# Optimization experiments

Hardware: AMD Instinct MI355X
Metric: run time of the kernel (lower is better)

The kernel has to match this reference:

```python
import jax, jax.numpy as jnp
import numpy as np

TEMP = 0.7
TOPK_RATIO = 0.75
BN_EPS = 1e-5  # eval-mode BN with running_mean=0, running_var=1


def conv3x3(x, w):
    # x: [N,C,H,W], w: [O,I,3,3], stride 1, pad 1
    return jax.lax.conv_general_dilated(x, w, (1, 1), 'SAME',
                                        dimension_numbers=('NCHW', 'OIHW', 'NCHW'))


def bn(x, g, b):
    scale = g / jnp.sqrt(1.0 + BN_EPS)
    return x * scale[:, None, None] + b[:, None, None]


def glu(x):
    c = x.shape[1] // 2
    return x[:, :c] * jax.nn.sigmoid(x[:, c:])


def resblock(x, w1, g1, b1, w2, g2, b2):
    out = glu(bn(conv3x3(x, w1), g1, b1))
    out = bn(conv3x3(out, w2), g2, b2)
    return out + x


def refined_attention(h_code, word_embs, w_ctx, mask):
    B, C, H, W = h_code.shape
    Q = H * W
    S = word_embs.shape[2]
    # conv_context is a 1x1 conv (no bias): pure channel projection
    sourceT = jnp.einsum('oc,bcs->bos', w_ctx, word_embs)   # [B, idf, S]
    target = h_code.reshape(B, C, Q)                        # [B, idf, Q]
    attn = jnp.einsum('bcq,bcs->bqs', target, sourceT)      # [B, Q, S]
    attn = attn.reshape(B * Q, S) / TEMP
    # faithful to torch: mask.repeat(queryL, 1) tiles mask over rows
    mask_exp = jnp.tile(mask, (Q, 1))                       # [B*Q, S]
    attn = jnp.where(mask_exp, -jnp.inf, attn)
    if TOPK_RATIO < 1.0 and S > 1:
        k = max(1, int(S * TOPK_RATIO))
        topk_vals, _ = jax.lax.top_k(attn, k)               # sorted desc
        threshold = topk_vals[:, -1:]                       # min of top-k
        attn = jnp.where(attn < threshold, -jnp.inf, attn)
    p = jax.nn.softmax(attn, axis=1)
    nan_rows = jnp.any(jnp.isnan(p), axis=1, keepdims=True)
    p = jnp.where(nan_rows, 1.0 / S, p)                     # uniform fallback
    p = p.reshape(B, Q, S)
    attn_t = jnp.swapaxes(p, 1, 2)                          # [B, S, Q]
    wctx = jnp.einsum('bos,bsq->boq', sourceT, attn_t).reshape(B, C, H, W)
    att_map = attn_t.reshape(B, S, H, W)
    return wctx, att_map


def upsample2x(x):
    return jnp.repeat(jnp.repeat(x, 2, axis=2), 2, axis=3)


def reference(h_code, c_code, word_embs, w_ctx,
              r0_w1, r0_g1, r0_b1, r0_w2, r0_g2, r0_b2,
              r1_w1, r1_g1, r1_b1, r1_w2, r1_g2, r1_b2,
              up_w, up_g, up_b, mask):
    # c_code is in the signature of NEXT_STAGE_G.forward but unused (as in AttnGAN)
    c_code_att, att = refined_attention(h_code, word_embs, w_ctx, mask)
    h_c = jnp.concatenate([h_code, c_code_att], axis=1)     # [B, 2*ngf, H, W]
    out = resblock(h_c, r0_w1, r0_g1, r0_b1, r0_w2, r0_g2, r0_b2)
    out = resblock(out, r1_w1, r1_g1, r1_b1, r1_w2, r1_g2, r1_b2)
    # upBlock: nearest upsample x2 -> conv3x3(2ngf, 2ngf) -> BN -> GLU -> ngf
    out = glu(bn(conv3x3(upsample2x(out), up_w), up_g, up_b))
    return out, att


def setup_inputs() -> dict:
    key = jax.random.key(0)
    ks = jax.random.split(key, 24)
    B, ngf, H, W = 8, 64, 128, 128
    nef, ncf, S = 256, 100, 32
    C2 = 2 * ngf  # 128
    std = 0.02
    inp = {
        'h_code': jax.random.normal(ks[0], (B, ngf, H, W), jnp.float32),
        'c_code': jax.random.normal(ks[1], (B, ncf), jnp.float32),
        'word_embs': jax.random.normal(ks[2], (B, nef, S), jnp.float32),
        'mask': jax.random.randint(ks[3], (B, S), 0, 2).astype(bool),
        'w_ctx': jax.random.normal(ks[4], (ngf, nef), jnp.float32) * std,
    }
    for i, base in enumerate([5, 11]):
        inp[f'r{i}_w1'] = jax.random.normal(ks[base + 0], (2 * C2, C2, 3, 3), jnp.float32) * std
        inp[f'r{i}_g1'] = jnp.ones((2 * C2,), jnp.float32)
        inp[f'r{i}_b1'] = jnp.zeros((2 * C2,), jnp.float32)
        inp[f'r{i}_w2'] = jax.random.normal(ks[base + 3], (C2, C2, 3, 3), jnp.float32) * std
        inp[f'r{i}_g2'] = jnp.ones((C2,), jnp.float32)
        inp[f'r{i}_b2'] = jnp.zeros((C2,), jnp.float32)
    inp['up_w'] = jax.random.normal(ks[17], (2 * ngf, C2, 3, 3), jnp.float32) * std
    inp['up_g'] = jnp.ones((2 * ngf,), jnp.float32)
    inp['up_b'] = jnp.zeros((2 * ngf,), jnp.float32)
    return inp
```

## Files before the change

kernel.cpp:

```cpp
#include <hip/hip_runtime.h>
#include <math.h>


#define B_N 8
#define NGF 64
#define HC 128
#define WC 128
#define QN (HC*WC)
#define NEF 256
#define SN 32
#define TEMP_INV (1.0f/0.7f)
#define BN_SC 0.99999500003749969f
#define TOPK 24

typedef _Float16 f16;
typedef __attribute__((ext_vector_type(8))) _Float16 f16x8;
typedef __attribute__((ext_vector_type(4))) _Float16 f16x4;
typedef __attribute__((ext_vector_type(4))) float f32x4;

__device__ __forceinline__ void gload16(const void* g, void* l) {
    __builtin_amdgcn_global_load_lds(
        (const __attribute__((address_space(1))) void*)g,
        (__attribute__((address_space(3))) void*)l,
        16, 0, 0);
}

__global__ void prep_mask_k(const void* __restrict__ mraw,
                            unsigned* __restrict__ mbits,
                            unsigned* __restrict__ zp) {
    __shared__ int mode;
    if (threadIdx.x == 0) {
        const unsigned* u = (const unsigned*)mraw;
        bool i32 = true, f32m = true;
        for (int i = 0; i < 64; ++i) {
            unsigned v = u[i];
            if (v > 1u) i32 = false;
            if (v != 0u && v != 0x3F800000u) f32m = false;
        }
        mode = i32 ? 0 : (f32m ? 1 : 2);
    }
    __syncthreads();
    int t = threadIdx.x;
    if (t < 64) zp[t] = 0u;
    if (t < B_N) {
        unsigned bits = 0;
        for (int s = 0; s < SN; ++s) {
            int idx = t * SN + s;
            bool on;
            if (mode == 0)      on = ((const int*)mraw)[idx] != 0;
            else if (mode == 1) on = ((const float*)mraw)[idx] != 0.0f;
            else                on = ((const unsigned char*)mraw)[idx] != 0;
            if (on) bits |= (1u << s);
        }
        mbits[t] = bits;
    }
}

__global__ __launch_bounds__(256) void source_t_k(
        const float* __restrict__ w_ctx, const float* __restrict__ word_embs,
        float* __restrict__ sT) {
    int b = blockIdx.x >> 3;
    int o = ((blockIdx.x & 7) << 3) + (threadIdx.x >> 5);
    int s = threadIdx.x & 31;
    const float* wrow = w_ctx + (size_t)o * NEF;
    const float* wb = word_embs + (size_t)b * NEF * SN + s;
    float acc = 0.0f;
    #pragma unroll 8
    for (int c = 0; c < NEF; ++c) acc += wrow[c] * wb[(size_t)c * SN];
    sT[((size_t)b * NGF + o) * SN + s] = acc;
}

__global__ __launch_bounds__(256) void attention_k(
        const float* __restrict__ h_code, const float* __restrict__ sT,
        const unsigned* __restrict__ mbits,
        float* __restrict__ att_out,
        f16* __restrict__ hc) {
    int r0 = blockIdx.x * 256;
    int b = r0 >> 14;
    __shared__ float st[NGF * SN];
    const float* stg = sT + (size_t)b * NGF * SN;
    for (int i = threadIdx.x; i < NGF * SN; i += 256) st[i] = stg[i];
    __syncthreads();
    int q = (r0 & (QN - 1)) + threadIdx.x;

    const float* hb = h_code + (size_t)b * NGF * QN + q;
    f16* hcb = hc + ((size_t)b * QN + q) * 128;

    float a[SN];
    #pragma unroll
    for (int s = 0; s < SN; ++s) a[s] = 0.0f;
    for (int c0 = 0; c0 < NGF; c0 += 4) {
        float v[4];
        f16x4 t;
        #pragma unroll
        for (int r = 0; r < 4; ++r) {
            v[r] = hb[(size_t)(c0 + r) * QN];
            t[r] = (f16)v[r];
            #pragma unroll
            for (int s = 0; s < SN; ++s) a[s] += v[r] * st[(c0 + r) * SN + s];
        }
        *(f16x4*)(hcb + c0) = t;
    }
    unsigned mb = mbits[q & 7];
    #pragma unroll
    for (int s = 0; s < SN; ++s)
        a[s] = ((mb >> s) & 1u) ? -INFINITY : a[s] * TEMP_INV;

    float thr = -INFINITY;
    #pragma unroll
    for (int s = 0; s < SN; ++s) {
        int rank = 0;
        #pragma unroll
        for (int j = 0; j < SN; ++j)
            rank += (a[j] > a[s]) || (a[j] == a[s] && j < s);
        if (rank == TOPK - 1) thr = a[s];
    }
    float m = -INFINITY;
    #pragma unroll
    for (int s = 0; s < SN; ++s) {
        if (a[s] < thr) a[s] = -INFINITY;
        m = fmaxf(m, a[s]);
    }
    float p[SN];
    if (m == -INFINITY) {
        #pragma unroll
        for (int s = 0; s < SN; ++s) p[s] = 1.0f / SN;
    } else {
        float sum = 0.0f;
        #pragma unroll
        for (int s = 0; s < SN; ++s) { p[s] = __expf(a[s] - m); sum += p[s]; }
        float inv = 1.0f / sum;
        #pragma unroll
        for (int s = 0; s < SN; ++s) p[s] *= inv;
    }
    float* ao = att_out + (size_t)b * SN * QN + q;
    #pragma unroll
    for (int s = 0; s < SN; ++s) ao[(size_t)s * QN] = p[s];
    for (int c0 = 0; c0 < NGF; c0 += 4) {
        f16x4 t;
        #pragma unroll
        for (int r = 0; r < 4; ++r) {
            float acc = 0.0f;
            #pragma unroll
            for (int s = 0; s < SN; ++s) acc += st[(c0 + r) * SN + s] * p[s];
            t[r] = (f16)acc;
        }
        *(f16x4*)(hcb + 64 + c0) = t;
    }
}

__global__ __launch_bounds__(256) void wt_transform_k(
        const float* __restrict__ w, f16* __restrict__ wt,
        int total, int HALF ) {
    int idx = blockIdx.x * 256 + threadIdx.x;
    if (idx >= total) return;
    int e   = idx & 7;
    int gp  = (idx >> 3) & 3;
    int cop = (idx >> 5) & 63;
    int u   = idx >> 11;
    int t   = u % 9;
    int v   = u / 9;
    int cc  = v & 3;
    int cb  = v >> 2;
    int g   = gp ^ ((cop >> 1) & 3);
    int ci  = cc * 32 + g * 8 + e;
    int co  = HALF ? (cop < 32 ? cb * 32 + cop : HALF + cb * 32 + (cop - 32))
                   : cb * 64 + cop;
    wt[idx] = (f16)w[((size_t)co * 128 + ci) * 9 + t];
}

__global__ __launch_bounds__(256) void wt_up_transform_k(
        const float* __restrict__ w, f16* __restrict__ wt) {
    int idx = blockIdx.x * 256 + threadIdx.x;
    int e   = idx & 7;
    int gp  = (idx >> 3) & 3;
    int cop = (idx >> 5) & 63;
    int tap = (idx >> 11) & 3;
    int pw  = (idx >> 13) & 1;
    int cc  = (idx >> 14) & 3;
    int ph  = (idx >> 16) & 1;
    int cb  = (idx >> 17) & 1;
    int g   = gp ^ ((cop >> 1) & 3);
    int ci  = cc * 32 + g * 8 + e;
    int co  = cop < 32 ? cb * 32 + cop : 64 + cb * 32 + (cop - 32);
    int ra = tap >> 1, bb = tap & 1;
    const float* wp = w + ((size_t)co * 128 + ci) * 9;
    float acc = 0.0f;
    #pragma unroll
    for (int kh = 0; kh < 3; ++kh) {
        int rma = (ph == 0) ? (kh == 0 ? 0 : 1) : (kh == 2 ? 1 : 0);
        if (rma != ra) continue;
        #pragma unroll
        for (int kw = 0; kw < 3; ++kw) {
            int cma = (pw == 0) ? (kw == 0 ? 0 : 1) : (kw == 2 ? 1 : 0);
            if (cma == bb) acc += wp[kh * 3 + kw];
        }
    }
    wt[idx] = (f16)acc;
}

template<int COUT, bool GLU, bool RES, bool UP, int HOUT, int WOUT, bool FINAL>
__global__ __launch_bounds__(256) void conv_mfma_k(
        const f16* __restrict__ in, const f16* __restrict__ wt,
        const float* __restrict__ gamma, const float* __restrict__ beta,
        const f16* __restrict__ res, f16* __restrict__ outh,
        float* __restrict__ outf, const char* __restrict__ zeros) {
    constexpr int HALF = COUT / 2;
    constexpr int OCH  = GLU ? HALF : COUT;
    constexpr int HIN  = UP ? HOUT / 2 : HOUT;
    constexpr int WIN  = UP ? WOUT / 2 : WOUT;
    constexpr int RPT  = 256 / WOUT;
    constexpr int ROWS_IN = UP ? 2 : RPT + 2;
    constexpr int NIN_G   = ROWS_IN * 520;
    constexpr int NIN_IT  = (NIN_G + 255) / 256;
    constexpr int NIN_PAD = NIN_IT * 256;
    constexpr int NTAP    = UP ? 4 : 9;
    constexpr int WBYTES  = UP ? 32768 : 36864;
    constexpr int WIT     = WBYTES / 4096;

    __shared__ char smem[NIN_PAD * 16 + WBYTES];
    char* sW = smem + NIN_PAD * 16;

    const int tid = threadIdx.x, lane = tid & 63, wv = tid >> 6;
    const int l15 = lane & 15, kg = lane >> 4;
    const int b = blockIdx.z, cb = blockIdx.y, qt = blockIdx.x;
    const int q0 = qt * 256;
    const int h0 = q0 / WOUT;
    const int ph = UP ? (h0 & 1) : 0;
    const int p  = wv >> 1;
    const int jq = ((wv & 1) << 6) + l15;

    f32x4 acc[4][4];
    #pragma unroll
    for (int m = 0; m < 4; ++m)
        #pragma unroll
        for (int n = 0; n < 4; ++n) acc[m][n] = (f32x4){0.f, 0.f, 0.f, 0.f};

    const f16* inb = in + (size_t)b * HIN * WIN * 128;
    const char* wtb = UP
        ? (const char*)wt + (size_t)(cb * 2 + ph) * 131072
        : (const char*)wt + (size_t)cb * 147456;

    const char* srcK[NIN_IT];
    #pragma unroll
    for (int k = 0; k < NIN_IT; ++k) {
        int idx = (k << 8) + tid;
        int r = idx / 520;
        int rem = idx - r * 520;
        int wi = rem >> 2, gp = rem & 3;
        int g = gp ^ ((wi >> 1) & 3);
        const char* s = zeros;
        if (UP) {
            int sh = (h0 >> 1) + r - 1 + ph;
            int sw = wi - 1;
            if (r < 2 && (unsigned)sh < (unsigned)HIN && (unsigned)sw < (unsigned)WIN)
                s = (const char*)(inb + (((size_t)sh * WIN + sw) << 7) + g * 8);
        } else {
            int gh = h0 - 1 + r;
            int gw = wi - 1;
            if (r < ROWS_IN && (unsigned)gh < (unsigned)HOUT && (unsigned)gw < (unsigned)WOUT)
                s = (const char*)(inb + (((size_t)gh * WIN + gw) << 7) + g * 8);
        }
        srcK[k] = s;
    }
    const int dstB = (tid & 192) << 4;

    for (int cc = 0; cc < 4; ++cc) {
        #pragma unroll
        for (int k = 0; k < NIN_IT; ++k)
            gload16(srcK[k] + cc * 64, smem + (k << 12) + dstB);
        const char* wsrc = wtb + cc * WBYTES + (tid << 4);
        #pragma unroll
        for (int k = 0; k < WIT; ++k)
            gload16(wsrc + (k << 12), sW + (k << 12) + dstB);
        __syncthreads();

        #pragma unroll
        for (int t = 0; t < NTAP; ++t) {
            f16x8 af[4], bf[4];
            const int tapbase = UP ? ((p * 4 + t) << 12) : (t << 12);
            #pragma unroll
            for (int m = 0; m < 4; ++m) {
                int co = m * 16 + l15;
                af[m] = *(const f16x8*)(sW + tapbase + (co << 6)
                                        + ((kg ^ ((co >> 1) & 3)) << 4));
            }
            #pragma unroll
            for (int n = 0; n < 4; ++n) {
                int off;
                if (UP) {
                    int si = jq + (n << 4) + (t & 1) + p;
                    off = (t >> 1) * 8320 + si * 64 + ((kg ^ ((si >> 1) & 3)) << 4);
                } else {
                    const int kh = t / 3, kw = t % 3;
                    int row = (wv >> 1) + kh;
                    int wi = ((wv & 1) << 6) + (n << 4) + l15 + kw;
                    off = row * 8320 + wi * 64 + ((kg ^ ((wi >> 1) & 3)) << 4);
                }
                bf[n] = *(const f16x8*)(smem + off);
            }
            #pragma unroll
            for (int m = 0; m < 4; ++m)
                #pragma unroll
                for (int n = 0; n < 4; ++n)
                    acc[m][n] = __builtin_amdgcn_mfma_f32_16x16x32_f16(af[m], bf[n], acc[m][n], 0, 0, 0);
        }
        __syncthreads();
    }

    const int r4 = kg * 4;
    if (GLU) {
        #pragma unroll
        for (int mv = 0; mv < 2; ++mv) {
            const int v0 = cb * 32 + mv * 16 + r4;
            float s1[4], o1[4], s2[4], o2[4];
            #pragma unroll
            for (int r = 0; r < 4; ++r) {
                s1[r] = gamma[v0 + r] * BN_SC;        o1[r] = beta[v0 + r];
                s2[r] = gamma[v0 + r + HALF] * BN_SC; o2[r] = beta[v0 + r + HALF];
            }
            #pragma unroll
            for (int n = 0; n < 4; ++n) {
                float ov[4];
                #pragma unroll
                for (int r = 0; r < 4; ++r) {
                    float yv = acc[mv][n][r] * s1[r] + o1[r];
                    float zv = acc[mv + 2][n][r] * s2[r] + o2[r];
                    ov[r] = yv / (1.0f + __expf(-zv));
                }
                if (FINAL) {
                    const int w = UP ? 2 * (jq + (n << 4)) + p
                                     : ((wv << 6) + (n << 4) + l15) % WOUT;
                    const int h = UP ? h0 : h0 + ((wv << 6) + (n << 4) + l15) / WOUT;
                    #pragma unroll
                    for (int r = 0; r < 4; ++r)
                        outf[(((size_t)b * OCH + v0 + r) * HOUT + h) * WOUT + w] = ov[r];
                } else {
                    const int qc = (wv << 6) + (n << 4) + l15;
                    f16x4 tv;
                    #pragma unroll
                    for (int r = 0; r < 4; ++r) tv[r] = (f16)ov[r];
                    *(f16x4*)(outh + ((size_t)b * HOUT * WOUT + q0 + qc) * OCH + v0) = tv;
                }
            }
        }
    } else {
        #pragma unroll
        for (int m = 0; m < 4; ++m) {
            const int c0 = cb * 64 + m * 16 + r4;
            float s[4], o[4];
            #pragma unroll
            for (int r = 0; r < 4; ++r) {
                s[r] = gamma[c0 + r] * BN_SC; o[r] = beta[c0 + r];
            }
            #pragma unroll
            for (int n = 0; n < 4; ++n) {
                const int qc = (wv << 6) + (n << 4) + l15;
                const size_t pix = (size_t)b * HOUT * WOUT + q0 + qc;
                float ov[4];
                #pragma unroll
                for (int r = 0; r < 4; ++r) ov[r] = acc[m][n][r] * s[r] + o[r];
                if (RES) {
                    f16x4 rv = *(const f16x4*)(res + pix * 128 + c0);
                    #pragma unroll
                    for (int r = 0; r < 4; ++r) ov[r] += (float)rv[r];
                }
                f16x4 tv;
                #pragma unroll
                for (int r = 0; r < 4; ++r) tv[r] = (f16)ov[r];
                *(f16x4*)(outh + pix * OCH + c0) = tv;
            }
        }
    }
}

extern "C" void kernel_launch(void* const* d_in, const int* in_sizes, int n_in,
                              void* d_out, int out_size, void* d_ws, size_t ws_size,
                              hipStream_t stream) {
    (void)in_sizes; (void)n_in; (void)out_size; (void)ws_size;
    const float* h_code    = (const float*)d_in[0];
    const float* word_embs = (const float*)d_in[2];
    const void*  mask      = d_in[3];
    const float* w_ctx     = (const float*)d_in[4];
    const float* r0_w1 = (const float*)d_in[5];
    const float* r0_g1 = (const float*)d_in[6];
    const float* r0_b1 = (const float*)d_in[7];
    const float* r0_w2 = (const float*)d_in[8];
    const float* r0_g2 = (const float*)d_in[9];
    const float* r0_b2 = (const float*)d_in[10];
    const float* r1_w1 = (const float*)d_in[11];
    const float* r1_g1 = (const float*)d_in[12];
    const float* r1_b1 = (const float*)d_in[13];
    const float* r1_w2 = (const float*)d_in[14];
    const float* r1_g2 = (const float*)d_in[15];
    const float* r1_b2 = (const float*)d_in[16];
    const float* up_w  = (const float*)d_in[17];
    const float* up_g  = (const float*)d_in[18];
    const float* up_b  = (const float*)d_in[19];

    float* outp = (float*)d_out;
    float* attp = outp + (size_t)B_N * NGF * 4 * HC * WC;

    unsigned* mbits = (unsigned*)d_ws;
    char* zeros = (char*)d_ws + 256;
    float* sT  = (float*)((char*)d_ws + 1024);
    f16* hcA   = (f16*)((char*)d_ws + (size_t)(1 << 20));
    f16* wtbuf = (f16*)((char*)d_ws + (size_t)33 * (1 << 20));

    const int W1_TOT = 4 * 4 * 9 * 64 * 32;
    const int W2_TOT = 2 * 4 * 9 * 64 * 32;
    const int WUP_TOT = 2 * 2 * 4 * 2 * 4 * 64 * 32;
    f16* Wr0c1 = wtbuf;
    f16* Wr0c2 = Wr0c1 + W1_TOT;
    f16* Wr1c1 = Wr0c2 + W2_TOT;
    f16* Wr1c2 = Wr1c1 + W1_TOT;
    f16* Wup   = Wr1c2 + W2_TOT;

    f16* Bbuf = (f16*)d_out;
    f16* Cbuf = (f16*)((char*)d_out + ((size_t)32 << 20));

    prep_mask_k<<<1, 64, 0, stream>>>(mask, mbits, (unsigned*)zeros);
    source_t_k<<<64, 256, 0, stream>>>(w_ctx, word_embs, sT);

    wt_transform_k<<<(W1_TOT + 255) / 256, 256, 0, stream>>>(r0_w1, Wr0c1, W1_TOT, 128);
    wt_transform_k<<<(W2_TOT + 255) / 256, 256, 0, stream>>>(r0_w2, Wr0c2, W2_TOT, 0);
    wt_transform_k<<<(W1_TOT + 255) / 256, 256, 0, stream>>>(r1_w1, Wr1c1, W1_TOT, 128);
    wt_transform_k<<<(W2_TOT + 255) / 256, 256, 0, stream>>>(r1_w2, Wr1c2, W2_TOT, 0);
    wt_up_transform_k<<<WUP_TOT / 256, 256, 0, stream>>>(up_w, Wup);

    attention_k<<<(B_N * QN) / 256, 256, 0, stream>>>(h_code, sT, mbits, attp, hcA);

    conv_mfma_k<256, true,  false, false, 128, 128, false>
        <<<dim3(64, 4, B_N), 256, 0, stream>>>(hcA, Wr0c1, r0_g1, r0_b1, nullptr, Bbuf, nullptr, zeros);
    conv_mfma_k<128, false, true,  false, 128, 128, false>
        <<<dim3(64, 2, B_N), 256, 0, stream>>>(Bbuf, Wr0c2, r0_g2, r0_b2, hcA, Cbuf, nullptr, zeros);
    conv_mfma_k<256, true,  false, false, 128, 128, false>
        <<<dim3(64, 4, B_N), 256, 0, stream>>>(Cbuf, Wr1c1, r1_g1, r1_b1, nullptr, Bbuf, nullptr, zeros);
    conv_mfma_k<128, false, true,  false, 128, 128, false>
        <<<dim3(64, 2, B_N), 256, 0, stream>>>(Bbuf, Wr1c2, r1_g2, r1_b2, Cbuf, hcA, nullptr, zeros);
    conv_mfma_k<128, true,  false, true,  256, 256, true>
        <<<dim3(256, 2, B_N), 256, 0, stream>>>(hcA, Wup, up_g, up_b, nullptr, nullptr, outp, zeros);
}
```

Baseline: 455.2 us.

## Switch intermediate activations to channel-group-planar f16 layout

Activation buffers between the attention kernel and the convolution kernels move from pixel-major NHWC with 128 channels to a blocked layout: 16 planes of 8 channels, each plane pixel-contiguous. Conv input gathers now step between channel chunks by plane offsets instead of 64-byte offsets, and epilogue stores and residual reads use the new addressing. The zero-padding region is relocated and zeroed at strided offsets so it can serve the new cc stride. The goal is more contiguous, coalesced global accesses for the 16-byte LDS-direct loads and the stores, at the risk of partial-line writes in the epilogues.

```diff
diff --git a/kernel.cpp b/kernel.cpp
--- a/kernel.cpp
+++ b/kernel.cpp
@@ -41,7 +41,7 @@
     }
     __syncthreads();
     int t = threadIdx.x;
-    if (t < 64) zp[t] = 0u;
+    if (t < 64) zp[(t >> 4) * 262144 + (t & 15)] = 0u;
     if (t < B_N) {
         unsigned bits = 0;
         for (int s = 0; s < SN; ++s) {
@@ -84,22 +84,21 @@
     int q = (r0 & (QN - 1)) + threadIdx.x;
 
     const float* hb = h_code + (size_t)b * NGF * QN + q;
-    f16* hcb = hc + ((size_t)b * QN + q) * 128;
+    f16* hcb = hc + (size_t)b * QN * 128;
 
     float a[SN];
     #pragma unroll
     for (int s = 0; s < SN; ++s) a[s] = 0.0f;
-    for (int c0 = 0; c0 < NGF; c0 += 4) {
-        float v[4];
-        f16x4 t;
-        #pragma unroll
-        for (int r = 0; r < 4; ++r) {
-            v[r] = hb[(size_t)(c0 + r) * QN];
-            t[r] = (f16)v[r];
-            #pragma unroll
-            for (int s = 0; s < SN; ++s) a[s] += v[r] * st[(c0 + r) * SN + s];
-        }
-        *(f16x4*)(hcb + c0) = t;
+    for (int g8 = 0; g8 < 8; ++g8) {
+        f16x8 t;
+        #pragma unroll
+        for (int r = 0; r < 8; ++r) {
+            float v = hb[(size_t)(g8 * 8 + r) * QN];
+            t[r] = (f16)v;
+            #pragma unroll
+            for (int s = 0; s < SN; ++s) a[s] += v * st[(g8 * 8 + r) * SN + s];
+        }
+        *(f16x8*)(hcb + ((size_t)g8 * QN + q) * 8) = t;
     }
     unsigned mb = mbits[q & 7];
     #pragma unroll
@@ -136,16 +135,16 @@
     float* ao = att_out + (size_t)b * SN * QN + q;
     #pragma unroll
     for (int s = 0; s < SN; ++s) ao[(size_t)s * QN] = p[s];
-    for (int c0 = 0; c0 < NGF; c0 += 4) {
-        f16x4 t;
-        #pragma unroll
-        for (int r = 0; r < 4; ++r) {
+    for (int g8 = 0; g8 < 8; ++g8) {
+        f16x8 t;
+        #pragma unroll
+        for (int r = 0; r < 8; ++r) {
             float acc = 0.0f;
             #pragma unroll
-            for (int s = 0; s < SN; ++s) acc += st[(c0 + r) * SN + s] * p[s];
+            for (int s = 0; s < SN; ++s) acc += st[(g8 * 8 + r) * SN + s] * p[s];
             t[r] = (f16)acc;
         }
-        *(f16x4*)(hcb + 64 + c0) = t;
+        *(f16x8*)(hcb + ((size_t)(8 + g8) * QN + q) * 8) = t;
     }
 }
 
@@ -254,12 +253,12 @@
             int sh = (h0 >> 1) + r - 1 + ph;
             int sw = wi - 1;
             if (r < 2 && (unsigned)sh < (unsigned)HIN && (unsigned)sw < (unsigned)WIN)
-                s = (const char*)(inb + (((size_t)sh * WIN + sw) << 7) + g * 8);
+                s = (const char*)(inb + (((size_t)g * (HIN * WIN) + (size_t)sh * WIN + sw) << 3));
         } else {
             int gh = h0 - 1 + r;
             int gw = wi - 1;
             if (r < ROWS_IN && (unsigned)gh < (unsigned)HOUT && (unsigned)gw < (unsigned)WOUT)
-                s = (const char*)(inb + (((size_t)gh * WIN + gw) << 7) + g * 8);
+                s = (const char*)(inb + (((size_t)g * (HIN * WIN) + (size_t)gh * WIN + gw) << 3));
         }
         srcK[k] = s;
     }
@@ -268,7 +267,7 @@
     for (int cc = 0; cc < 4; ++cc) {
         #pragma unroll
         for (int k = 0; k < NIN_IT; ++k)
-            gload16(srcK[k] + cc * 64, smem + (k << 12) + dstB);
+            gload16(srcK[k] + (cc << 20), smem + (k << 12) + dstB);
         const char* wsrc = wtb + cc * WBYTES + (tid << 4);
         #pragma unroll
         for (int k = 0; k < WIT; ++k)
@@ -340,7 +339,8 @@
                     f16x4 tv;
                     #pragma unroll
                     for (int r = 0; r < 4; ++r) tv[r] = (f16)ov[r];
-                    *(f16x4*)(outh + ((size_t)b * HOUT * WOUT + q0 + qc) * OCH + v0) = tv;
+                    *(f16x4*)(outh + ((((size_t)b * (OCH / 8) + (v0 >> 3)) << 14)
+                                      + q0 + qc) * 8 + (v0 & 7)) = tv;
                 }
             }
         }
@@ -356,19 +356,19 @@
             #pragma unroll
             for (int n = 0; n < 4; ++n) {
                 const int qc = (wv << 6) + (n << 4) + l15;
-                const size_t pix = (size_t)b * HOUT * WOUT + q0 + qc;
+                const size_t gaddr = ((((size_t)b * 16 + (c0 >> 3)) << 14) + q0 + qc) * 8 + (c0 & 7);
                 float ov[4];
                 #pragma unroll
                 for (int r = 0; r < 4; ++r) ov[r] = acc[m][n][r] * s[r] + o[r];
                 if (RES) {
-                    f16x4 rv = *(const f16x4*)(res + pix * 128 + c0);
+                    f16x4 rv = *(const f16x4*)(res + gaddr);
                     #pragma unroll
                     for (int r = 0; r < 4; ++r) ov[r] += (float)rv[r];
                 }
                 f16x4 tv;
                 #pragma unroll
                 for (int r = 0; r < 4; ++r) tv[r] = (f16)ov[r];
-                *(f16x4*)(outh + pix * OCH + c0) = tv;
+                *(f16x4*)(outh + gaddr) = tv;
             }
         }
     }
@@ -402,10 +402,10 @@
     float* attp = outp + (size_t)B_N * NGF * 4 * HC * WC;
 
     unsigned* mbits = (unsigned*)d_ws;
-    char* zeros = (char*)d_ws + 256;
     float* sT  = (float*)((char*)d_ws + 1024);
-    f16* hcA   = (f16*)((char*)d_ws + (size_t)(1 << 20));
-    f16* wtbuf = (f16*)((char*)d_ws + (size_t)33 * (1 << 20));
+    char* zeros = (char*)d_ws + ((size_t)4 << 20);
+    f16* hcA   = (f16*)((char*)d_ws + ((size_t)8 << 20));
+    f16* wtbuf = (f16*)((char*)d_ws + ((size_t)40 << 20));
 
     const int W1_TOT = 4 * 4 * 9 * 64 * 32;
     const int W2_TOT = 2 * 4 * 9 * 64 * 32;
```

Result: faster. 404.3 us (-11.2%).
